# Performance work log

Hardware: AMD Instinct MI355X
Metric: run time of the kernel (lower is better)

## Reference

```python
import jax, jax.numpy as jnp
import numpy as np

LOG_2PI = float(np.log(2.0 * np.pi))


def setup_inputs() -> dict:
    key = jax.random.key(0)
    k1, k2, k3, k4 = jax.random.split(key, 4)
    B, Tin, Tout, D = 32, 512, 2048, 256
    memory = jax.random.normal(k1, (B, Tin, D), dtype=jnp.float32)
    # durations in [1, 7) frames per token (mean ~4 -> ~Tout total frames)
    duration = jax.random.uniform(k2, (B, Tin), dtype=jnp.float32) * 6.0 + 1.0
    # positive Gaussian widths in [0.5, 2.0)
    sigma = jax.random.uniform(k3, (B, Tin), dtype=jnp.float32) * 1.5 + 0.5
    output_lengths = jnp.full((B,), Tout, dtype=jnp.int32)
    mask = jax.random.uniform(k4, (B, Tin)) < 0.1
    return {"memory": memory, "duration": duration, "sigma": sigma,
            "output_lengths": output_lengths, "mask": mask}


def reference(memory, duration, sigma, output_lengths, mask):
    # memory: (B,Tin,D); duration,sigma,mask: (B,Tin); output_lengths: (B,)
    Tout = int(np.max(np.asarray(output_lengths)))
    frames = jnp.arange(Tout, dtype=jnp.float32)[None, None, :]          # (1,1,Tout)
    center = jnp.cumsum(duration, axis=-1) - 0.5 * duration              # (B,Tin)
    c = center[..., None]                                                # (B,Tin,1)
    s = sigma[..., None]                                                 # (B,Tin,1)
    # Normal(loc=c, scale=s).log_prob(frames).exp()
    z = (frames - c) / s
    alignment = jnp.exp(-0.5 * z * z - jnp.log(s) - 0.5 * LOG_2PI)       # (B,Tin,Tout)
    alignment = jnp.where(mask[..., None], 0.0, alignment)               # masked_fill
    attn_weights = alignment / (jnp.sum(alignment, axis=1, keepdims=True) + 1e-8)
    # bmm(attn^T, memory): (B,Tout,Tin) @ (B,Tin,D) -> (B,Tout,D)
    upsampled = jnp.einsum('bit,bid->btd', attn_weights, memory)
    return upsampled, attn_weights
```

## Files before the change

kernel.cpp:

```cpp
#include <hip/hip_runtime.h>
#include <hip/hip_bf16.h>
#include <math.h>

#define HALF_LOG_2PI 0.9189385332046727f
#define WIN 32.0f
#define TILE_T 4

__global__ void detect_mask_mode_k(const unsigned int* __restrict__ mw,
                                   int nwords, int* __restrict__ mode) {
    __shared__ int s_not[2];
    if (threadIdx.x == 0) { s_not[0] = 0; s_not[1] = 0; }
    __syncthreads();
    int notInt = 0, notF32 = 0;
    for (int i = threadIdx.x; i < nwords; i += blockDim.x) {
        unsigned int w = mw[i];
        notInt |= (w != 0u && w != 1u);
        notF32 |= (w != 0u && w != 0x3F800000u);
    }
    if (notInt) atomicOr(&s_not[0], 1);
    if (notF32) atomicOr(&s_not[1], 1);
    __syncthreads();
    if (threadIdx.x == 0)
        *mode = (!s_not[0]) ? 0 : ((!s_not[1]) ? 1 : 2);
}

__global__ void prep_k(const float* __restrict__ duration,
                       const float* __restrict__ sigma,
                       const void* __restrict__ mask,
                       const int* __restrict__ mode_p,
                       float* __restrict__ center,
                       float* __restrict__ amp,
                       float* __restrict__ inv_sigma,
                       int Tin) {
    __shared__ float s[1024];
    int b = blockIdx.x;
    int i = threadIdx.x;
    size_t gi = (size_t)b * Tin + i;
    float d = duration[gi];
    s[i] = d;
    __syncthreads();
    for (int off = 1; off < Tin; off <<= 1) {
        float v = (i >= off) ? s[i - off] : 0.0f;
        __syncthreads();
        s[i] += v;
        __syncthreads();
    }
    float c = s[i] - 0.5f * d;
    int mode = *mode_p;
    bool m;
    if (mode == 0)      m = ((const int*)mask)[gi] != 0;
    else if (mode == 1) m = ((const float*)mask)[gi] != 0.0f;
    else                m = ((const unsigned char*)mask)[gi] != 0;
    float sg = sigma[gi];
    center[gi]    = c;
    inv_sigma[gi] = 1.0f / sg;
    amp[gi]       = m ? 0.0f : __expf(-__logf(sg) - HALF_LOG_2PI);
}

__global__ __launch_bounds__(256) void denom_k(
        const float* __restrict__ center, const float* __restrict__ amp,
        const float* __restrict__ inv_sigma,
        float* __restrict__ denom, int* __restrict__ lo_out,
        int* __restrict__ cnt_out, int Tin, int Tout) {
    __shared__ float sc[1024], sa[1024], si[1024];
    int b = blockIdx.y;
    int t = blockIdx.x * 256 + threadIdx.x;
    for (int i = threadIdx.x; i < Tin; i += 256) {
        size_t g = (size_t)b * Tin + i;
        sc[i] = center[g]; sa[i] = amp[g]; si[i] = inv_sigma[g];
    }
    __syncthreads();
    if (t >= Tout) return;
    float tf = (float)t;
    int lo = 0, hi = Tin;
    while (lo < hi) {
        int mid = (lo + hi) >> 1;
        if (sc[mid] < tf - WIN) lo = mid + 1; else hi = mid;
    }
    float sum = 0.0f;
    int i = lo;
    for (; i < Tin; ++i) {
        float c = sc[i];
        if (c > tf + WIN) break;
        float z = (tf - c) * si[i];
        sum += sa[i] * __expf(-0.5f * z * z);
    }
    size_t g = (size_t)b * Tout + t;
    denom[g]   = sum + 1e-8f;
    lo_out[g]  = lo;
    cnt_out[g] = i - lo;
}

__global__ __launch_bounds__(256) void attn_k(
        const float* __restrict__ center, const float* __restrict__ amp,
        const float* __restrict__ inv_sigma, const float* __restrict__ denom,
        float* __restrict__ attn, int Tin, int Tout) {
    int bi = blockIdx.x;
    int b = bi / Tin;
    float c = center[bi], a = amp[bi], inv = inv_sigma[bi];
    const float* den = denom + (size_t)b * Tout;
    float* row = attn + (size_t)bi * Tout;
    for (int t4 = threadIdx.x * 4; t4 < Tout; t4 += 256 * 4) {
        float r[4];
        if ((float)(t4 + 3) < c - WIN || (float)t4 > c + WIN) {
            r[0] = r[1] = r[2] = r[3] = 0.0f;
        } else {
            #pragma unroll
            for (int j = 0; j < 4; ++j) {
                float tf = (float)(t4 + j);
                float dlt = tf - c;
                if (fabsf(dlt) < WIN) {
                    float z = dlt * inv;
                    r[j] = a * __expf(-0.5f * z * z) / den[t4 + j];
                } else {
                    r[j] = 0.0f;
                }
            }
        }
        *(float4*)(row + t4) = make_float4(r[0], r[1], r[2], r[3]);
    }
}

__global__ __launch_bounds__(256) void upsample_k(
        const float* __restrict__ mem, const float* __restrict__ center,
        const float* __restrict__ amp, const float* __restrict__ inv_sigma,
        const float* __restrict__ denom, const int* __restrict__ lo_ws,
        const int* __restrict__ cnt_ws, float* __restrict__ out,
        int Tin, int Tout, int D) {
    __shared__ float w_s[TILE_T][128];
    __shared__ int s_lo, s_cnt;
    int nwg = gridDim.x;
    int wid = blockIdx.x;
    int work = wid;
    if ((nwg & 7) == 0) {
        int chunk = nwg >> 3;
        work = (wid & 7) * chunk + (wid >> 3);
    }
    int tpb = Tout / TILE_T;
    int b  = work / tpb;
    int t0 = (work % tpb) * TILE_T;
    int tid = threadIdx.x;
    if (tid == 0) {
        int lo0 = lo_ws[(size_t)b * Tout + t0];
        size_t g3 = (size_t)b * Tout + t0 + TILE_T - 1;
        int hi = lo_ws[g3] + cnt_ws[g3];
        s_lo = lo0;
        s_cnt = hi - lo0;
    }
    __syncthreads();
    int lo0 = s_lo;
    int wcnt = s_cnt;
    if (wcnt > 128) wcnt = 128;
    #pragma unroll
    for (int rep = 0; rep < 2; ++rep) {
        int id = tid + rep * 256;
        int f = id >> 7;
        int w = id & 127;
        float wgt = 0.0f;
        int i = lo0 + w;
        if (w < wcnt && i < Tin) {
            float tf = (float)(t0 + f);
            size_t gi = (size_t)b * Tin + i;
            float c = center[gi];
            float dlt = tf - c;
            if (fabsf(dlt) < WIN) {
                float z = dlt * inv_sigma[gi];
                wgt = amp[gi] * __expf(-0.5f * z * z)
                      / denom[(size_t)b * Tout + t0 + f];
            }
        }
        w_s[f][w] = wgt;
    }
    __syncthreads();
    for (int d = tid; d < D; d += 256) {
        float acc0 = 0.f, acc1 = 0.f, acc2 = 0.f, acc3 = 0.f;
        const float* mrow = mem + ((size_t)b * Tin + lo0) * D + d;
        for (int w = 0; w < wcnt; ++w) {
            float m = mrow[(size_t)w * D];
            acc0 += w_s[0][w] * m;
            acc1 += w_s[1][w] * m;
            acc2 += w_s[2][w] * m;
            acc3 += w_s[3][w] * m;
        }
        float* orow = out + ((size_t)b * Tout + t0) * D + d;
        orow[0]          = acc0;
        orow[(size_t)D]  = acc1;
        orow[2*(size_t)D] = acc2;
        orow[3*(size_t)D] = acc3;
    }
}

extern "C" void kernel_launch(void* const* d_in, const int* in_sizes, int n_in,
                              void* d_out, int out_size, void* d_ws, size_t ws_size,
                              hipStream_t stream) {
    const float* memory   = (const float*)d_in[0];
    const float* duration = (const float*)d_in[1];
    const float* sigma    = (const float*)d_in[2];
    const void* mask = d_in[4];

    int B   = in_sizes[3];
    int Tin = in_sizes[1] / B;
    int D   = in_sizes[0] / (B * Tin);
    int Tout = out_size / (B * (D + Tin));

    float* out_up   = (float*)d_out;
    float* out_attn = out_up + (size_t)B * Tout * D;

    char* w = (char*)d_ws;
    int*   mode   = (int*)w;
    float* center = (float*)(w + 256);
    float* amp    = center + (size_t)B * Tin;
    float* inv    = amp    + (size_t)B * Tin;
    float* den    = inv    + (size_t)B * Tin;
    int*   lo     = (int*)(den + (size_t)B * Tout);
    int*   cnt    = lo + (size_t)B * Tout;

    detect_mask_mode_k<<<1, 256, 0, stream>>>(
        (const unsigned int*)mask, (B * Tin) / 4, mode);
    prep_k<<<B, Tin, 0, stream>>>(duration, sigma, mask, mode,
                                  center, amp, inv, Tin);
    denom_k<<<dim3((Tout + 255) / 256, B), 256, 0, stream>>>(
        center, amp, inv, den, lo, cnt, Tin, Tout);
    attn_k<<<B * Tin, 256, 0, stream>>>(center, amp, inv, den,
                                        out_attn, Tin, Tout);
    upsample_k<<<(B * Tout) / TILE_T, 256, 0, stream>>>(
        memory, center, amp, inv, den, lo, cnt, out_up, Tin, Tout, D);
}
```

Baseline: 72.89 us.

## Fuse prep/denom and attn/upsample kernels, enlarge time tile, use nontemporal stores

Cuts the launch sequence from five kernels to two. Mask-mode detection, the prefix sum and the denominator computation are merged into one per-batch kernel. The attention-row writes and the upsample GEMV are merged into one grid whose blocks are interleaved 4:1, so the write-heavy and compute-heavy work run at the same time. The upsample tile grows from 4 to 16 output frames so each memory row is reused more, the denominator is stored as a reciprocal to avoid divisions, and the large outputs use nontemporal stores. In exchange, every prep block redundantly scans the whole mask, and there are fewer, heavier upsample blocks with more register pressure.

```diff
diff --git a/kernel.cpp b/kernel.cpp
--- a/kernel.cpp
+++ b/kernel.cpp
@@ -4,189 +4,180 @@
 
 #define HALF_LOG_2PI 0.9189385332046727f
 #define WIN 32.0f
-#define TILE_T 4
-
-__global__ void detect_mask_mode_k(const unsigned int* __restrict__ mw,
-                                   int nwords, int* __restrict__ mode) {
+#define TILE_T 16
+
+typedef float f32x4 __attribute__((ext_vector_type(4)));
+
+__global__ __launch_bounds__(1024) void prep_denom_k(
+        const float* __restrict__ duration, const float* __restrict__ sigma,
+        const void* __restrict__ mask,
+        float* __restrict__ center, float* __restrict__ amp,
+        float* __restrict__ inv_sigma, float* __restrict__ inv_den,
+        int* __restrict__ lo_ws, int* __restrict__ cnt_ws,
+        int B, int Tin, int Tout) {
+    __shared__ float sc[1024], sa[1024], si[1024];
     __shared__ int s_not[2];
-    if (threadIdx.x == 0) { s_not[0] = 0; s_not[1] = 0; }
-    __syncthreads();
-    int notInt = 0, notF32 = 0;
-    for (int i = threadIdx.x; i < nwords; i += blockDim.x) {
-        unsigned int w = mw[i];
-        notInt |= (w != 0u && w != 1u);
-        notF32 |= (w != 0u && w != 0x3F800000u);
-    }
-    if (notInt) atomicOr(&s_not[0], 1);
-    if (notF32) atomicOr(&s_not[1], 1);
-    __syncthreads();
-    if (threadIdx.x == 0)
-        *mode = (!s_not[0]) ? 0 : ((!s_not[1]) ? 1 : 2);
-}
-
-__global__ void prep_k(const float* __restrict__ duration,
-                       const float* __restrict__ sigma,
-                       const void* __restrict__ mask,
-                       const int* __restrict__ mode_p,
-                       float* __restrict__ center,
-                       float* __restrict__ amp,
-                       float* __restrict__ inv_sigma,
-                       int Tin) {
-    __shared__ float s[1024];
-    int b = blockIdx.x;
-    int i = threadIdx.x;
-    size_t gi = (size_t)b * Tin + i;
+    int b = blockIdx.x, tid = threadIdx.x;
+    if (tid < 2) s_not[tid] = 0;
+    __syncthreads();
+    {
+        const unsigned int* mw = (const unsigned int*)mask;
+        int nwords = (B * Tin) >> 2;
+        int nI = 0, nF = 0;
+        for (int i = tid; i < nwords; i += blockDim.x) {
+            unsigned int w = mw[i];
+            nI |= (w != 0u && w != 1u);
+            nF |= (w != 0u && w != 0x3F800000u);
+        }
+        if (nI) atomicOr(&s_not[0], 1);
+        if (nF) atomicOr(&s_not[1], 1);
+    }
+    size_t gi = (size_t)b * Tin + tid;
     float d = duration[gi];
-    s[i] = d;
+    sc[tid] = d;
     __syncthreads();
     for (int off = 1; off < Tin; off <<= 1) {
-        float v = (i >= off) ? s[i - off] : 0.0f;
+        float v = (tid >= off) ? sc[tid - off] : 0.0f;
         __syncthreads();
-        s[i] += v;
+        sc[tid] += v;
         __syncthreads();
     }
-    float c = s[i] - 0.5f * d;
-    int mode = *mode_p;
+    float c = sc[tid] - 0.5f * d;
+    int mode = s_not[0] ? (s_not[1] ? 2 : 1) : 0;
     bool m;
     if (mode == 0)      m = ((const int*)mask)[gi] != 0;
     else if (mode == 1) m = ((const float*)mask)[gi] != 0.0f;
     else                m = ((const unsigned char*)mask)[gi] != 0;
     float sg = sigma[gi];
-    center[gi]    = c;
-    inv_sigma[gi] = 1.0f / sg;
-    amp[gi]       = m ? 0.0f : __expf(-__logf(sg) - HALF_LOG_2PI);
+    float a  = m ? 0.0f : __expf(-__logf(sg) - HALF_LOG_2PI);
+    float is = 1.0f / sg;
+    center[gi] = c; amp[gi] = a; inv_sigma[gi] = is;
+    sc[tid] = c; sa[tid] = a; si[tid] = is;
+    __syncthreads();
+    for (int t = tid; t < Tout; t += blockDim.x) {
+        float tf = (float)t;
+        int lo = 0, hi = Tin;
+        while (lo < hi) {
+            int mid = (lo + hi) >> 1;
+            if (sc[mid] < tf - WIN) lo = mid + 1; else hi = mid;
+        }
+        float sum = 0.0f;
+        int i = lo;
+        for (; i < Tin; ++i) {
+            float cc = sc[i];
+            if (cc > tf + WIN) break;
+            float z = (tf - cc) * si[i];
+            sum += sa[i] * __expf(-0.5f * z * z);
+        }
+        size_t g = (size_t)b * Tout + t;
+        inv_den[g] = 1.0f / (sum + 1e-8f);
+        lo_ws[g]   = lo;
+        cnt_ws[g]  = i - lo;
+    }
 }
 
-__global__ __launch_bounds__(256) void denom_k(
-        const float* __restrict__ center, const float* __restrict__ amp,
-        const float* __restrict__ inv_sigma,
-        float* __restrict__ denom, int* __restrict__ lo_out,
-        int* __restrict__ cnt_out, int Tin, int Tout) {
-    __shared__ float sc[1024], sa[1024], si[1024];
-    int b = blockIdx.y;
-    int t = blockIdx.x * 256 + threadIdx.x;
-    for (int i = threadIdx.x; i < Tin; i += 256) {
-        size_t g = (size_t)b * Tin + i;
-        sc[i] = center[g]; sa[i] = amp[g]; si[i] = inv_sigma[g];
-    }
-    __syncthreads();
-    if (t >= Tout) return;
-    float tf = (float)t;
-    int lo = 0, hi = Tin;
-    while (lo < hi) {
-        int mid = (lo + hi) >> 1;
-        if (sc[mid] < tf - WIN) lo = mid + 1; else hi = mid;
-    }
-    float sum = 0.0f;
-    int i = lo;
-    for (; i < Tin; ++i) {
-        float c = sc[i];
-        if (c > tf + WIN) break;
-        float z = (tf - c) * si[i];
-        sum += sa[i] * __expf(-0.5f * z * z);
-    }
-    size_t g = (size_t)b * Tout + t;
-    denom[g]   = sum + 1e-8f;
-    lo_out[g]  = lo;
-    cnt_out[g] = i - lo;
-}
-
-__global__ __launch_bounds__(256) void attn_k(
-        const float* __restrict__ center, const float* __restrict__ amp,
-        const float* __restrict__ inv_sigma, const float* __restrict__ denom,
-        float* __restrict__ attn, int Tin, int Tout) {
-    int bi = blockIdx.x;
-    int b = bi / Tin;
-    float c = center[bi], a = amp[bi], inv = inv_sigma[bi];
-    const float* den = denom + (size_t)b * Tout;
-    float* row = attn + (size_t)bi * Tout;
-    for (int t4 = threadIdx.x * 4; t4 < Tout; t4 += 256 * 4) {
-        float r[4];
-        if ((float)(t4 + 3) < c - WIN || (float)t4 > c + WIN) {
-            r[0] = r[1] = r[2] = r[3] = 0.0f;
-        } else {
-            #pragma unroll
-            for (int j = 0; j < 4; ++j) {
-                float tf = (float)(t4 + j);
-                float dlt = tf - c;
-                if (fabsf(dlt) < WIN) {
-                    float z = dlt * inv;
-                    r[j] = a * __expf(-0.5f * z * z) / den[t4 + j];
-                } else {
-                    r[j] = 0.0f;
+__global__ __launch_bounds__(256) void attn_upsample_k(
+        const float* __restrict__ mem, const float* __restrict__ center,
+        const float* __restrict__ amp, const float* __restrict__ inv_sigma,
+        const float* __restrict__ inv_den, const int* __restrict__ lo_ws,
+        const int* __restrict__ cnt_ws, float* __restrict__ attn,
+        float* __restrict__ out, int nAttn, int nUp,
+        int Tin, int Tout, int D) {
+    __shared__ __align__(16) float w_s[TILE_T][128];
+    __shared__ float s_iden[TILE_T];
+    __shared__ int s_lo, s_cnt;
+    int bid = blockIdx.x;
+    int tid = threadIdx.x;
+    int aid = -1, uid = -1;
+    if (nAttn == 4 * nUp) {
+        int q = bid / 5, r = bid - q * 5;
+        if (r == 4) uid = q; else aid = q * 4 + r;
+    } else {
+        if (bid < nAttn) aid = bid; else uid = bid - nAttn;
+    }
+
+    if (aid >= 0) {
+        int bi = aid;
+        int b  = bi / Tin;
+        float c = center[bi], a = amp[bi], inv = inv_sigma[bi];
+        const float* iden = inv_den + (size_t)b * Tout;
+        float* row = attn + (size_t)bi * Tout;
+        for (int t4 = tid * 4; t4 < Tout; t4 += 256 * 4) {
+            f32x4 rv;
+            if ((float)(t4 + 3) < c - WIN || (float)t4 > c + WIN) {
+                rv = (f32x4)0.0f;
+            } else {
+                #pragma unroll
+                for (int j = 0; j < 4; ++j) {
+                    float dlt = (float)(t4 + j) - c;
+                    if (fabsf(dlt) < WIN) {
+                        float z = dlt * inv;
+                        rv[j] = a * __expf(-0.5f * z * z) * iden[t4 + j];
+                    } else rv[j] = 0.0f;
                 }
             }
-        }
-        *(float4*)(row + t4) = make_float4(r[0], r[1], r[2], r[3]);
-    }
-}
-
-__global__ __launch_bounds__(256) void upsample_k(
-        const float* __restrict__ mem, const float* __restrict__ center,
-        const float* __restrict__ amp, const float* __restrict__ inv_sigma,
-        const float* __restrict__ denom, const int* __restrict__ lo_ws,
-        const int* __restrict__ cnt_ws, float* __restrict__ out,
-        int Tin, int Tout, int D) {
-    __shared__ float w_s[TILE_T][128];
-    __shared__ int s_lo, s_cnt;
-    int nwg = gridDim.x;
-    int wid = blockIdx.x;
-    int work = wid;
-    if ((nwg & 7) == 0) {
-        int chunk = nwg >> 3;
-        work = (wid & 7) * chunk + (wid >> 3);
-    }
+            __builtin_nontemporal_store(rv, (f32x4*)(row + t4));
+        }
+        return;
+    }
+
     int tpb = Tout / TILE_T;
-    int b  = work / tpb;
-    int t0 = (work % tpb) * TILE_T;
-    int tid = threadIdx.x;
+    int b   = uid / tpb;
+    int t0  = (uid - b * tpb) * TILE_T;
     if (tid == 0) {
-        int lo0 = lo_ws[(size_t)b * Tout + t0];
-        size_t g3 = (size_t)b * Tout + t0 + TILE_T - 1;
-        int hi = lo_ws[g3] + cnt_ws[g3];
-        s_lo = lo0;
-        s_cnt = hi - lo0;
-    }
-    __syncthreads();
-    int lo0 = s_lo;
-    int wcnt = s_cnt;
-    if (wcnt > 128) wcnt = 128;
+        size_t g0 = (size_t)b * Tout + t0;
+        size_t g1 = g0 + (TILE_T - 1);
+        int lo0 = lo_ws[g0];
+        int cnt = lo_ws[g1] + cnt_ws[g1] - lo0;
+        s_lo  = lo0;
+        s_cnt = cnt > 128 ? 128 : cnt;
+    }
+    if (tid < TILE_T) s_iden[tid] = inv_den[(size_t)b * Tout + t0 + tid];
+    __syncthreads();
+    int lo0 = s_lo, wcnt = s_cnt;
     #pragma unroll
-    for (int rep = 0; rep < 2; ++rep) {
+    for (int rep = 0; rep < (TILE_T * 128) / 256; ++rep) {
         int id = tid + rep * 256;
-        int f = id >> 7;
-        int w = id & 127;
+        int f = id >> 7, w = id & 127;
         float wgt = 0.0f;
         int i = lo0 + w;
         if (w < wcnt && i < Tin) {
-            float tf = (float)(t0 + f);
             size_t gi = (size_t)b * Tin + i;
-            float c = center[gi];
-            float dlt = tf - c;
+            float dlt = (float)(t0 + f) - center[gi];
             if (fabsf(dlt) < WIN) {
                 float z = dlt * inv_sigma[gi];
-                wgt = amp[gi] * __expf(-0.5f * z * z)
-                      / denom[(size_t)b * Tout + t0 + f];
+                wgt = amp[gi] * __expf(-0.5f * z * z) * s_iden[f];
             }
         }
         w_s[f][w] = wgt;
     }
     __syncthreads();
     for (int d = tid; d < D; d += 256) {
-        float acc0 = 0.f, acc1 = 0.f, acc2 = 0.f, acc3 = 0.f;
+        float acc[TILE_T];
+        #pragma unroll
+        for (int f = 0; f < TILE_T; ++f) acc[f] = 0.0f;
         const float* mrow = mem + ((size_t)b * Tin + lo0) * D + d;
-        for (int w = 0; w < wcnt; ++w) {
-            float m = mrow[(size_t)w * D];
-            acc0 += w_s[0][w] * m;
-            acc1 += w_s[1][w] * m;
-            acc2 += w_s[2][w] * m;
-            acc3 += w_s[3][w] * m;
+        int w4 = wcnt & ~3;
+        for (int w = 0; w < w4; w += 4) {
+            float m0 = mrow[(size_t)(w + 0) * D];
+            float m1 = mrow[(size_t)(w + 1) * D];
+            float m2 = mrow[(size_t)(w + 2) * D];
+            float m3 = mrow[(size_t)(w + 3) * D];
+            #pragma unroll
+            for (int f = 0; f < TILE_T; ++f) {
+                f32x4 wv = *(const f32x4*)&w_s[f][w];
+                acc[f] += wv.x * m0 + wv.y * m1 + wv.z * m2 + wv.w * m3;
+            }
+        }
+        for (int w = w4; w < wcnt; ++w) {
+            float m0 = mrow[(size_t)w * D];
+            #pragma unroll
+            for (int f = 0; f < TILE_T; ++f) acc[f] += w_s[f][w] * m0;
         }
         float* orow = out + ((size_t)b * Tout + t0) * D + d;
-        orow[0]          = acc0;
-        orow[(size_t)D]  = acc1;
-        orow[2*(size_t)D] = acc2;
-        orow[3*(size_t)D] = acc3;
+        #pragma unroll
+        for (int f = 0; f < TILE_T; ++f)
+            __builtin_nontemporal_store(acc[f], orow + (size_t)f * D);
     }
 }
 
@@ -196,33 +187,29 @@
     const float* memory   = (const float*)d_in[0];
     const float* duration = (const float*)d_in[1];
     const float* sigma    = (const float*)d_in[2];
-    const void* mask = d_in[4];
-
-    int B   = in_sizes[3];
-    int Tin = in_sizes[1] / B;
-    int D   = in_sizes[0] / (B * Tin);
+    const void*  mask     = d_in[4];
+
+    int B    = in_sizes[3];
+    int Tin  = in_sizes[1] / B;
+    int D    = in_sizes[0] / (B * Tin);
     int Tout = out_size / (B * (D + Tin));
 
     float* out_up   = (float*)d_out;
     float* out_attn = out_up + (size_t)B * Tout * D;
 
-    char* w = (char*)d_ws;
-    int*   mode   = (int*)w;
-    float* center = (float*)(w + 256);
+    float* center = (float*)d_ws;
     float* amp    = center + (size_t)B * Tin;
     float* inv    = amp    + (size_t)B * Tin;
-    float* den    = inv    + (size_t)B * Tin;
-    int*   lo     = (int*)(den + (size_t)B * Tout);
+    float* iden   = inv    + (size_t)B * Tin;
+    int*   lo     = (int*)(iden + (size_t)B * Tout);
     int*   cnt    = lo + (size_t)B * Tout;
 
-    detect_mask_mode_k<<<1, 256, 0, stream>>>(
-        (const unsigned int*)mask, (B * Tin) / 4, mode);
-    prep_k<<<B, Tin, 0, stream>>>(duration, sigma, mask, mode,
-                                  center, amp, inv, Tin);
-    denom_k<<<dim3((Tout + 255) / 256, B), 256, 0, stream>>>(
-        center, amp, inv, den, lo, cnt, Tin, Tout);
-    attn_k<<<B * Tin, 256, 0, stream>>>(center, amp, inv, den,
-                                        out_attn, Tin, Tout);
-    upsample_k<<<(B * Tout) / TILE_T, 256, 0, stream>>>(
-        memory, center, amp, inv, den, lo, cnt, out_up, Tin, Tout, D);
+    prep_denom_k<<<B, Tin, 0, stream>>>(duration, sigma, mask,
+                                        center, amp, inv, iden, lo, cnt,
+                                        B, Tin, Tout);
+    int nAttn = B * Tin;
+    int nUp   = (B * Tout) / TILE_T;
+    attn_upsample_k<<<nAttn + nUp, 256, 0, stream>>>(
+        memory, center, amp, inv, iden, lo, cnt,
+        out_attn, out_up, nAttn, nUp, Tin, Tout, D);
 }
```

New measurement: 82.82 us. +13.6%, slower.
